# Performance work log

Measured on AMD Instinct MI355X. Metric: run time of the kernel, lower is better.

## Reference

```python
import jax, jax.numpy as jnp
import numpy as np

QLEN, BSZ, HID, NH, HD = 512, 8, 1024, 16, 64
PLEN = 2 * QLEN
SCALE = 1.0 / (HD ** 0.5)
BIG_NUM = 1e30
EPS = 1e-5


def _rel_shift(x, klen):
    # x: [b, n, i, j] -> shifted [b, n, i, klen], same raw-reshape trick as torch.
    b, n, i, j = x.shape
    x = x.reshape(b, n, j, i)[:, :, 1:, :]
    x = x.reshape(b, n, i, j - 1)
    return x[:, :, :, :klen]


def setup_inputs() -> dict:
    key = jax.random.key(0)
    ks = jax.random.split(key, 12)
    s = jnp.float32(0.02)
    return {
        "hidden_states": jax.random.normal(ks[0], (QLEN, BSZ, HID), jnp.float32),
        "position_embed": jax.random.normal(ks[1], (PLEN, BSZ, HID), jnp.float32),
        "segment_embed": jax.random.uniform(ks[2], (QLEN, QLEN, BSZ, 2), jnp.float32),
        "attn_mask": jnp.zeros((QLEN, QLEN, BSZ, 1), jnp.float32),
        "q": jax.random.normal(ks[3], (HID, NH, HD), jnp.float32) * s,
        "k": jax.random.normal(ks[4], (HID, NH, HD), jnp.float32) * s,
        "v": jax.random.normal(ks[5], (HID, NH, HD), jnp.float32) * s,
        "r": jax.random.normal(ks[6], (HID, NH, HD), jnp.float32) * s,
        "o": jax.random.normal(ks[7], (HID, NH, HD), jnp.float32) * s,
        "r_w_bias": jax.random.normal(ks[8], (NH, HD), jnp.float32) * s,
        "r_r_bias": jax.random.normal(ks[9], (NH, HD), jnp.float32) * s,
        "r_s_bias": jax.random.normal(ks[10], (NH, HD), jnp.float32) * s,
        "seg_mat": jax.random.normal(ks[11], (2, NH, HD), jnp.float32) * s,
        "ln_gamma": jnp.ones((HID,), jnp.float32),
        "ln_beta": jnp.zeros((HID,), jnp.float32),
    }


def reference(hidden_states, position_embed, segment_embed, attn_mask,
              q, k, v, r, o, r_w_bias, r_r_bias, r_s_bias, seg_mat,
              ln_gamma, ln_beta):
    query = jnp.einsum('ibh,hnd->ibnd', hidden_states, q)
    key_ = jnp.einsum('ibh,hnd->ibnd', hidden_states, k)
    value = jnp.einsum('ibh,hnd->ibnd', hidden_states, v)
    key_r = jnp.einsum('ibh,hnd->ibnd', position_embed, r)

    # content score
    ac = jnp.einsum('ibnd,jbnd->bnij', query + r_w_bias, key_)
    # relative position score with rel_shift
    bd = jnp.einsum('ibnd,jbnd->bnij', query + r_r_bias, key_r)
    bd = _rel_shift(bd, ac.shape[3])
    # segment score
    ef = jnp.einsum('ibnd,snd->ibns', query + r_s_bias, seg_mat)
    ef = jnp.einsum('ijbs,ibns->bnij', segment_embed, ef)

    attn_score = (ac + bd + ef) * SCALE
    attn_score = attn_score - BIG_NUM * jnp.transpose(attn_mask, (2, 3, 0, 1))
    attn_prob = jax.nn.softmax(attn_score, axis=-1)  # dropout is identity in eval

    attn_out = jnp.einsum('bnij,jbnd->ibnd', attn_prob, value)
    attn_out = jnp.einsum('ibnd,hnd->ibh', attn_out, o)

    x = attn_out + hidden_states
    mu = jnp.mean(x, axis=-1, keepdims=True)
    var = jnp.mean((x - mu) ** 2, axis=-1, keepdims=True)
    return (x - mu) * jax.lax.rsqrt(var + EPS) * ln_gamma + ln_beta
```

## Files before the change

kernel.cpp:

```cpp
#include <hip/hip_runtime.h>
#include <hip/hip_bf16.h>

#define I_LEN 512
#define BSZ   8
#define HIDN  1024
#define NHEAD 16
#define HDIM  64
#define PLEN_ 1024
#define SCALE_F 0.125f
#define BIGNUM 1e30f
#define LN_EPS 1e-5f

typedef unsigned int   u32;
typedef unsigned short u16;
typedef __attribute__((ext_vector_type(8))) short bf16x8;
typedef __attribute__((ext_vector_type(4))) float f32x4;

__device__ __forceinline__ float bflo(u32 w) { return __uint_as_float(w << 16); }
__device__ __forceinline__ float bfhi(u32 w) { return __uint_as_float(w & 0xffff0000u); }
__device__ __forceinline__ u16 f2bf(float x) {
  u32 u = __float_as_uint(x);
  return (u16)((u + 0x7fffu + ((u >> 16) & 1u)) >> 16);
}
__device__ __forceinline__ void bf8_to_f(const uint4 v, float* f) {
  f[0] = bflo(v.x); f[1] = bfhi(v.x);
  f[2] = bflo(v.y); f[3] = bfhi(v.y);
  f[4] = bflo(v.z); f[5] = bfhi(v.z);
  f[6] = bflo(v.w); f[7] = bfhi(v.w);
}

#define GLOAD_LDS16(gp, lp) __builtin_amdgcn_global_load_lds( \
    (const __attribute__((address_space(1))) void*)(gp),      \
    (__attribute__((address_space(3))) void*)(lp), 16, 0, 0)

__device__ __forceinline__ void setrans_body(int i, int j,
    const float* __restrict__ sege, const float* __restrict__ amask,
    u16* __restrict__ SE4, u16* __restrict__ MK) {
  const float* sp = &sege[((size_t)i * 512 + j) * 16];
  const float* mp = &amask[((size_t)i * 512 + j) * 8];
  float se[16], mk[8];
#pragma unroll
  for (int q = 0; q < 4; ++q) {
    const float4 f = *(const float4*)(sp + q * 4);
    se[q * 4 + 0] = f.x; se[q * 4 + 1] = f.y; se[q * 4 + 2] = f.z; se[q * 4 + 3] = f.w;
  }
#pragma unroll
  for (int q = 0; q < 2; ++q) {
    const float4 f = *(const float4*)(mp + q * 4);
    mk[q * 4 + 0] = f.x; mk[q * 4 + 1] = f.y; mk[q * 4 + 2] = f.z; mk[q * 4 + 3] = f.w;
  }
#pragma unroll
  for (int b = 0; b < 8; ++b) {
    const u32 pk = (u32)f2bf(se[b * 2]) | ((u32)f2bf(se[b * 2 + 1]) << 16);
    const size_t plane = ((size_t)b * 512 + i) * 512 + j;
    *(u32*)&SE4[plane * 2] = pk;
    MK[plane] = f2bf(BIGNUM * mk[b]);
  }
}

__global__ __launch_bounds__(256)
void prep_kernel(const float* __restrict__ W0, const float* __restrict__ W1,
                 const float* __restrict__ W2, const float* __restrict__ W3,
                 u16* __restrict__ T0, u16* __restrict__ T1,
                 u16* __restrict__ T2, u16* __restrict__ T3,
                 const float* __restrict__ hidden, const float* __restrict__ ow,
                 u16* __restrict__ Hb, u16* __restrict__ Wob,
                 const float* __restrict__ sege, const float* __restrict__ amask,
                 u16* __restrict__ SE4, u16* __restrict__ MK,
                 const float* __restrict__ pos, u16* __restrict__ Pb) {
  const int blk = blockIdx.x;
  const int t = threadIdx.x;
  if (blk >= 4608) {
    const size_t off = ((size_t)(blk - 4608) * 256 + t) * 8;
    const float4 a = *(const float4*)&pos[off];
    const float4 b = *(const float4*)&pos[off + 4];
    ushort4 o0, o1;
    o0.x = f2bf(a.x); o0.y = f2bf(a.y); o0.z = f2bf(a.z); o0.w = f2bf(a.w);
    o1.x = f2bf(b.x); o1.y = f2bf(b.y); o1.z = f2bf(b.z); o1.w = f2bf(b.w);
    *(ushort4*)&Pb[off] = o0;
    *(ushort4*)&Pb[off + 4] = o1;
    return;
  }
  if (blk >= 3584) {
    const int sid = blk - 3584;
    setrans_body(sid & 511, (sid >> 9) * 256 + t, sege, amask, SE4, MK);
    return;
  }
  if (blk >= 1024) {
    const size_t i = (size_t)(blk - 1024) * 256 + t;
    const float* src; u16* dst; size_t off;
    if (i < 524288) { src = hidden; dst = Hb;  off = i * 8; }
    else            { src = ow;     dst = Wob; off = (i - 524288) * 8; }
    const float4 a = *(const float4*)&src[off];
    const float4 b = *(const float4*)&src[off + 4];
    ushort4 o0, o1;
    o0.x = f2bf(a.x); o0.y = f2bf(a.y); o0.z = f2bf(a.z); o0.w = f2bf(a.w);
    o1.x = f2bf(b.x); o1.y = f2bf(b.y); o1.z = f2bf(b.z); o1.w = f2bf(b.w);
    *(ushort4*)&dst[off] = o0;
    *(ushort4*)&dst[off + 4] = o1;
    return;
  }
  __shared__ u16 tile[64][72];
  const int x = blk & 15, y = (blk >> 4) & 15, z = blk >> 8;
  const float* W = (z == 0) ? W0 : ((z == 1) ? W1 : ((z == 2) ? W2 : W3));
  u16* T = (z == 0) ? T0 : ((z == 1) ? T1 : ((z == 2) ? T2 : T3));
  const int h0 = y * 64, nd0 = x * 64;
  {
    const int hr = t >> 2, c0 = (t & 3) * 16;
#pragma unroll
    for (int q = 0; q < 4; ++q) {
      const float4 f = *(const float4*)&W[(size_t)(h0 + hr) * 1024 + nd0 + c0 + q * 4];
      tile[hr][c0 + q * 4 + 0] = f2bf(f.x);
      tile[hr][c0 + q * 4 + 1] = f2bf(f.y);
      tile[hr][c0 + q * 4 + 2] = f2bf(f.z);
      tile[hr][c0 + q * 4 + 3] = f2bf(f.w);
    }
  }
  __syncthreads();
  const int ndr = t >> 2, hc0 = (t & 3) * 16;
  union { u16 us[16]; uint4 qv[2]; } o;
#pragma unroll
  for (int e = 0; e < 16; ++e) o.us[e] = tile[hc0 + e][ndr];
  uint4* dst = (uint4*)&T[(size_t)(nd0 + ndr) * 1024 + h0 + hc0];
  dst[0] = o.qv[0]; dst[1] = o.qv[1];
}

__global__ __launch_bounds__(256)
void proj_gemm(const u16* __restrict__ Hb, const float* __restrict__ pos,
               const u16* __restrict__ Pb,
               const u16* __restrict__ Wqt, const u16* __restrict__ Wkt,
               const u16* __restrict__ Wvt, const u16* __restrict__ Wrt,
               u16* __restrict__ Qh, u16* __restrict__ Kf,
               u16* __restrict__ Vh, u16* __restrict__ Krf) {
  constexpr int K = 1024;
  __shared__ union {
    struct { u16 As[2 * 8192]; u16 Bs[2 * 8192]; } st;
    u16 epi[4][64 * 68];
    u16 epiK[128 * 137];
  } sm;
  u16* As = sm.st.As;
  u16* Bs = sm.st.Bs;
  const int id = blockIdx.x;
  const int low = id & 7;
  const int rest = id >> 3;
  const int bx = rest & 7;
  const int grp = low + 8 * (rest >> 3);
  const int by = grp & 31;
  const int z = grp >> 5;
  const u16* Bt; u16* C;
  if (z == 0)      { Bt = Wqt; C = Qh;  }
  else if (z == 1) { Bt = Wkt; C = Kf;  }
  else if (z == 2) { Bt = Wvt; C = Vh;  }
  else if (z == 3) { Bt = Wrt; C = Krf; }
  else             { Bt = Wrt; C = Krf; }
  const int rowoff = (z == 4) ? 4096 : 0;
  const float* Apos = pos + (size_t)rowoff * 1024;
  const u16* A16 = (z < 3) ? Hb : (Pb ? Pb + (size_t)rowoff * 1024 : nullptr);
  const int bm = by * 128, bn = bx * 128;
  const int tid = threadIdx.x, wv = tid >> 6, lane = tid & 63;
  const int l15 = lane & 15, g = lane >> 4;
  const int wr = wv >> 1, wc = wv & 1;

#define STAGE_B_P(BUF, K0)                                                    \
  _Pragma("unroll")                                                           \
  for (int p = 0; p < 4; ++p) {                                               \
    const int unit = (wv * 4 + p) * 64 + lane;                                \
    const int row = unit >> 3, up = unit & 7, cc = up ^ (row & 7);            \
    GLOAD_LDS16(&Bt[(size_t)(bn + row) * K + (K0) + cc * 8],                  \
                &Bs[(BUF) * 8192 + unit * 8]);                                \
  }
#define STAGE_A16_P(BUF, K0)                                                  \
  _Pragma("unroll")                                                           \
  for (int p = 0; p < 4; ++p) {                                               \
    const int unit = (wv * 4 + p) * 64 + lane;                                \
    const int row = unit >> 3, up = unit & 7, cc = up ^ (row & 7);            \
    GLOAD_LDS16(&A16[(size_t)(bm + row) * K + (K0) + cc * 8],                 \
                &As[(BUF) * 8192 + unit * 8]);                                \
  }
#define STAGE_A32_P(BUF, K0)                                                  \
  _Pragma("unroll")                                                           \
  for (int p = 0; p < 4; ++p) {                                               \
    const int unit = p * 256 + tid;                                           \
    const int row = unit >> 3, up = unit & 7, cc = up ^ (row & 7);            \
    const float* src = &Apos[(size_t)(bm + row) * K + (K0) + cc * 8];         \
    const float4 f0 = *(const float4*)src;                                    \
    const float4 f1 = *(const float4*)(src + 4);                              \
    ushort4 h0, h1;                                                           \
    h0.x = f2bf(f0.x); h0.y = f2bf(f0.y); h0.z = f2bf(f0.z); h0.w = f2bf(f0.w); \
    h1.x = f2bf(f1.x); h1.y = f2bf(f1.y); h1.z = f2bf(f1.z); h1.w = f2bf(f1.w); \
    *(ushort4*)&As[(BUF) * 8192 + unit * 8] = h0;                             \
    *(ushort4*)&As[(BUF) * 8192 + unit * 8 + 4] = h1;                         \
  }
#define COMPUTE_TILE(CUR)                                                     \
  {                                                                           \
    const u16* Ac = &As[(CUR) * 8192];                                        \
    const u16* Bc = &Bs[(CUR) * 8192];                                        \
    _Pragma("unroll")                                                         \
    for (int h = 0; h < 2; ++h) {                                             \
      bf16x8 af[4], bfv[4];                                                   \
      _Pragma("unroll")                                                       \
      for (int m = 0; m < 4; ++m) {                                           \
        const int row = wr * 64 + m * 16 + l15;                               \
        af[m] = *(const bf16x8*)&Ac[row * 64 + ((h * 4 + g) ^ (row & 7)) * 8];\
      }                                                                       \
      _Pragma("unroll")                                                       \
      for (int n = 0; n < 4; ++n) {                                           \
        const int col = wc * 64 + n * 16 + l15;                               \
        bfv[n] = *(const bf16x8*)&Bc[col * 64 + ((h * 4 + g) ^ (col & 7)) * 8];\
      }                                                                       \
      _Pragma("unroll")                                                       \
      for (int m = 0; m < 4; ++m)                                             \
        _Pragma("unroll")                                                     \
        for (int n = 0; n < 4; ++n)                                           \
          acc[m][n] = __builtin_amdgcn_mfma_f32_16x16x32_bf16(af[m], bfv[n],  \
                                                              acc[m][n], 0, 0, 0); \
    }                                                                         \
  }

  f32x4 acc[4][4];
#pragma unroll
  for (int m = 0; m < 4; ++m)
#pragma unroll
    for (int n = 0; n < 4; ++n) acc[m][n] = (f32x4){0.f, 0.f, 0.f, 0.f};

  if (A16) {
    STAGE_B_P(0, 0);
    STAGE_A16_P(0, 0);
    int cur = 0;
    for (int t = 0; t < 16; ++t) {
      if (t < 15) {
        const int k1 = (t + 1) * 64;
        STAGE_B_P(cur ^ 1, k1);
        STAGE_A16_P(cur ^ 1, k1);
        asm volatile("s_waitcnt vmcnt(8)" ::: "memory");
      } else {
        asm volatile("s_waitcnt vmcnt(0)" ::: "memory");
      }
      __builtin_amdgcn_s_barrier();
      __builtin_amdgcn_sched_barrier(0);
      COMPUTE_TILE(cur);
      __builtin_amdgcn_s_barrier();
      cur ^= 1;
    }
  } else {
    STAGE_B_P(0, 0);
    STAGE_A32_P(0, 0);
    __syncthreads();
    int cur = 0;
    for (int t = 0; t < 16; ++t) {
      if (t < 15) {
        const int k1 = (t + 1) * 64;
        STAGE_B_P(cur ^ 1, k1);
        STAGE_A32_P(cur ^ 1, k1);
      }
      COMPUTE_TILE(cur);
      __syncthreads();
      cur ^= 1;
    }
  }

  if (z == 1 || z >= 3) {
    u16* E128 = sm.epiK;
#pragma unroll
    for (int m = 0; m < 4; ++m)
#pragma unroll
      for (int nf = 0; nf < 4; ++nf)
#pragma unroll
        for (int r = 0; r < 4; ++r)
          E128[(wr * 64 + m * 16 + g * 4 + r) * 137 + wc * 64 + nf * 16 + l15] =
              f2bf(acc[m][nf][r]);
    __syncthreads();
    const int tK = (z == 1) ? by : (by + ((z == 4) ? 32 : 0));
    const int TS = (z == 1) ? 32 : 64;
#pragma unroll
    for (int q = 0; q < 8; ++q) {
      const int rid = wv * 8 + q;
      const int n_loc = rid >> 4, b_ = (rid >> 1) & 7, h = rid & 1;
      union { u16 us[8]; uint4 qv; } o;
#pragma unroll
      for (int e = 0; e < 8; ++e)
        o.us[e] = E128[(l15 * 8 + b_) * 137 + n_loc * 64 + h * 32 + g * 8 + e];
      const int head = bx * 2 + n_loc;
      const size_t base = (((size_t)(b_ * 16 + head) * TS + tK) * 2 + h) * 512 + lane * 8;
      *(uint4*)&C[base] = o.qv;
    }
  } else {
    u16* slice = sm.epi[wv];
    __syncthreads();
#pragma unroll
    for (int m = 0; m < 4; ++m)
#pragma unroll
      for (int nf = 0; nf < 4; ++nf)
#pragma unroll
        for (int r = 0; r < 4; ++r)
          slice[(m * 16 + g * 4 + r) * 68 + nf * 16 + l15] = f2bf(acc[m][nf][r]);
#pragma unroll
    for (int it = 0; it < 8; ++it) {
      const int rl = it * 8 + (lane >> 3);
      const int cl = (lane & 7) * 8;
      const ushort4 a = *(const ushort4*)&slice[rl * 68 + cl];
      const ushort4 b2 = *(const ushort4*)&slice[rl * 68 + cl + 4];
      const int row = bm + wr * 64 + rl;
      const int col = bn + wc * 64 + cl;
      const size_t idx = ((size_t)((row & 7) * 16 + (col >> 6)) * 512 + (row >> 3)) * 64 + (col & 63);
      *(ushort4*)&C[idx] = a;
      *(ushort4*)&C[idx + 4] = b2;
    }
  }
}

__global__ __launch_bounds__(256)
void post_kernel(u16* __restrict__ V, const u16* __restrict__ Qh,
                 const float* __restrict__ rsb, const float* __restrict__ segm,
                 float* __restrict__ E) {
  const int blk = blockIdx.x;
  const int t = threadIdx.x;
  if (blk >= 1024) {
    const int gt = (blk - 1024) * 256 + t;
    const int i = gt >> 7, bb = (gt >> 4) & 7, n = gt & 15;
    const size_t base = (((size_t)bb * 16 + n) * 512 + i) * 64;
    float e0 = 0.f, e1 = 0.f;
#pragma unroll
    for (int u8 = 0; u8 < 8; ++u8) {
      const uint4 qv = *(const uint4*)&Qh[base + u8 * 8];
      float qf[8];
      bf8_to_f(qv, qf);
#pragma unroll
      for (int w = 0; w < 8; ++w) {
        const int d = u8 * 8 + w;
        const float q = qf[w] + rsb[n * HDIM + d];
        e0 += q * segm[n * HDIM + d];
        e1 += q * segm[HIDN + n * HDIM + d];
      }
    }
    E[(size_t)gt * 2 + 0] = e0;
    E[(size_t)gt * 2 + 1] = e1;
    return;
  }
  __shared__ u16 tile[64][72];
  const int bn = blk & 127, slab = blk >> 7;
  const size_t base = ((size_t)bn * 8 + slab) * 4096;
  {
    const int jl = t >> 2, c0 = (t & 3) * 16;
    const uint4 v0 = *(const uint4*)&V[base + jl * 64 + c0];
    const uint4 v1 = *(const uint4*)&V[base + jl * 64 + c0 + 8];
    *(uint4*)&tile[jl][c0] = v0;
    *(uint4*)&tile[jl][c0 + 8] = v1;
  }
  __syncthreads();
  const int lane = t & 63, g = lane >> 4, l15 = lane & 15;
#pragma unroll
  for (int w = 0; w < 2; ++w) {
    const int run = w * 4 + (t >> 6);
    const int c = run >> 1, h = run & 1;
    union { u16 us[8]; uint4 qv; } o;
#pragma unroll
    for (int e = 0; e < 8; ++e) o.us[e] = tile[h * 32 + g * 8 + e][16 * c + l15];
    *(uint4*)&V[base + run * 512 + lane * 8] = o.qv;
  }
}

__global__ __launch_bounds__(256)
void attn_mfma(const u16* __restrict__ Qh, const u16* __restrict__ Kf,
               const u16* __restrict__ Vf, const u16* __restrict__ Krf,
               const float* __restrict__ E, const u16* __restrict__ SE4,
               const u16* __restrict__ MK, const float* __restrict__ rwb,
               const float* __restrict__ rrb, u16* __restrict__ AOb) {
  __shared__ u16 Pl[4][16 * 64];
  const int id = blockIdx.x;
  const int b = id & 7, n = (id >> 3) & 15;
  const int i0 = (id >> 7) * 64;
  const int bn = b * 16 + n;
  const int t = threadIdx.x, wv = t >> 6, lane = t & 63;
  const int l15 = lane & 15, g = lane >> 4;
  const int irow0 = i0 + wv * 16;
  u16* Pw = Pl[wv];
  const int bn64 = bn * 64;

  bf16x8 qcf[2], qrf[2];
#pragma unroll
  for (int h = 0; h < 2; ++h) {
    const int d0 = 32 * h + g * 8;
    const uint4 qv = *(const uint4*)&Qh[((size_t)bn * 512 + irow0 + l15) * 64 + d0];
    float qf[8]; bf8_to_f(qv, qf);
    union { u16 us[8]; bf16x8 v; } ua, ub;
#pragma unroll
    for (int w = 0; w < 8; ++w) {
      ua.us[w] = f2bf((qf[w] + rwb[n * HDIM + d0 + w]) * SCALE_F);
      ub.us[w] = f2bf((qf[w] + rrb[n * HDIM + d0 + w]) * SCALE_F);
    }
    qcf[h] = ua.v; qrf[h] = ub.v;
  }

  float e0v[4], e1v[4], lrun[4];
  f32x4 accO[4];
#pragma unroll
  for (int r = 0; r < 4; ++r) {
    const int i = irow0 + 4 * g + r;
    const float2 ee = *(const float2*)&E[((size_t)(i * BSZ + b) * NHEAD + n) * 2];
    e0v[r] = ee.x * SCALE_F; e1v[r] = ee.y * SCALE_F;
    lrun[r] = 0.f;
  }
#pragma unroll
  for (int c = 0; c < 4; ++c) accO[c] = (f32x4){0.f, 0.f, 0.f, 0.f};

  for (int jb = 0; jb < I_LEN; jb += 64) {
    u32 sev[4][4]; u16 mkv[4][4];
#pragma unroll
    for (int c = 0; c < 4; ++c)
#pragma unroll
      for (int r = 0; r < 4; ++r) {
        const size_t plane = ((size_t)b * 512 + (irow0 + 4 * g + r)) * 512 + jb + 16 * c + l15;
        sev[c][r] = *(const u32*)&SE4[plane * 2];
        mkv[c][r] = MK[plane];
      }
    bf16x8 vf[4][2];
#pragma unroll
    for (int c = 0; c < 4; ++c) {
      const u16* vp = &Vf[((((size_t)bn * 8 + (jb >> 6)) * 4 + c) * 2) * 512 + lane * 8];
      vf[c][0] = *(const bf16x8*)vp;
      vf[c][1] = *(const bf16x8*)(vp + 512);
    }
    f32x4 S[4];
#pragma unroll
    for (int c = 0; c < 4; ++c) S[c] = (f32x4){0.f, 0.f, 0.f, 0.f};
#pragma unroll
    for (int c = 0; c < 4; ++c) {
      const u16* kp = &Kf[(((size_t)bn * 32 + (jb >> 4) + c) * 2) * 512 + lane * 8];
      S[c] = __builtin_amdgcn_mfma_f32_16x16x32_bf16(qcf[0], *(const bf16x8*)kp, S[c], 0, 0, 0);
      S[c] = __builtin_amdgcn_mfma_f32_16x16x32_bf16(qcf[1], *(const bf16x8*)(kp + 512), S[c], 0, 0, 0);
    }
    const int tb = (jb + 496 - irow0) >> 4;
    f32x4 T[5];
#pragma unroll
    for (int c = 0; c < 5; ++c) T[c] = (f32x4){0.f, 0.f, 0.f, 0.f};
#pragma unroll
    for (int c = 0; c < 5; ++c) {
      const u16* kp = &Krf[(((size_t)bn * 64 + tb + c) * 2) * 512 + lane * 8];
      T[c] = __builtin_amdgcn_mfma_f32_16x16x32_bf16(qrf[0], *(const bf16x8*)kp, T[c], 0, 0, 0);
      T[c] = __builtin_amdgcn_mfma_f32_16x16x32_bf16(qrf[1], *(const bf16x8*)(kp + 512), T[c], 0, 0, 0);
    }
    float bd[4][4];
#pragma unroll
    for (int r = 0; r < 4; ++r) {
      const int ii = 4 * g + r;
      const int pos_ = (lane & 48) | ((l15 - ii) & 15);
      float bp[5];
#pragma unroll
      for (int c = 0; c < 5; ++c) bp[c] = __shfl(T[c][r], pos_, 64);
      const bool sel = l15 >= ii;
#pragma unroll
      for (int c = 0; c < 4; ++c) bd[c][r] = sel ? bp[c + 1] : bp[c];
    }
#pragma unroll
    for (int c = 0; c < 4; ++c)
#pragma unroll
      for (int r = 0; r < 4; ++r) {
        const u32 sev_ = sev[c][r];
        const float s = S[c][r] + bd[c][r] + bflo(sev_) * e0v[r] + bfhi(sev_) * e1v[r]
                        - bflo((u32)mkv[c][r]);
        const float p = __expf(s);
        S[c][r] = p;
        lrun[r] += p;
      }
#pragma unroll
    for (int c = 0; c < 4; ++c)
#pragma unroll
      for (int r = 0; r < 4; ++r) {
        const int ii = 4 * g + r;
        Pw[ii * 64 + ((16 * c + l15) ^ ((ii & 7) << 3))] = f2bf(S[c][r]);
      }
    const bf16x8 pa0 = *(const bf16x8*)&Pw[l15 * 64 + ((g * 8) ^ ((l15 & 7) << 3))];
    const bf16x8 pa1 = *(const bf16x8*)&Pw[l15 * 64 + ((32 + g * 8) ^ ((l15 & 7) << 3))];
#pragma unroll
    for (int c = 0; c < 4; ++c) {
      accO[c] = __builtin_amdgcn_mfma_f32_16x16x32_bf16(pa0, vf[c][0], accO[c], 0, 0, 0);
      accO[c] = __builtin_amdgcn_mfma_f32_16x16x32_bf16(pa1, vf[c][1], accO[c], 0, 0, 0);
    }
  }
#pragma unroll
  for (int r = 0; r < 4; ++r) {
#pragma unroll
    for (int o = 1; o < 16; o <<= 1) lrun[r] += __shfl_xor(lrun[r], o);
  }
#pragma unroll
  for (int c = 0; c < 4; ++c)
#pragma unroll
    for (int r = 0; r < 4; ++r) {
      const int ii = 4 * g + r;
      AOb[(size_t)(irow0 + ii) * 8192 + bn64 + 16 * c + l15] = f2bf(accO[c][r] / lrun[r]);
    }
}

__global__ __launch_bounds__(256)
void oproj_gemm(const u16* __restrict__ A, const u16* __restrict__ Wob,
                const float* __restrict__ Res, float* __restrict__ C) {
  constexpr int K = 1024;
  __shared__ u16 As[2 * 4096];
  __shared__ u16 Bs[2 * 8192];
  const int id = blockIdx.x;
  const int low = id & 7;
  const int rest = id >> 3;
  const int bx = rest & 7;
  const int by = low + 8 * (rest >> 3);
  const int bm = by * 64, bn = bx * 128;
  const int tid = threadIdx.x, wv = tid >> 6, lane = tid & 63;
  const int l15 = lane & 15, g = lane >> 4;
  const int wr = wv >> 1, wc = wv & 1;

#define STAGE_O(BUF, K0)                                                      \
  _Pragma("unroll")                                                           \
  for (int p = 0; p < 2; ++p) {                                               \
    const int unit = (wv * 2 + p) * 64 + lane;                                \
    const int row = unit >> 3, up = unit & 7, cc = up ^ (row & 7);            \
    GLOAD_LDS16(&A[(size_t)(bm + row) * K + (K0) + cc * 8],                   \
                &As[(BUF) * 4096 + unit * 8]);                                \
  }                                                                           \
  _Pragma("unroll")                                                           \
  for (int p = 0; p < 4; ++p) {                                               \
    const int unit = (wv * 4 + p) * 64 + lane;                                \
    const int row = unit >> 3, up = unit & 7, cc = up ^ (row & 7);            \
    GLOAD_LDS16(&Wob[(size_t)(bn + row) * K + (K0) + cc * 8],                 \
                &Bs[(BUF) * 8192 + unit * 8]);                                \
  }

  f32x4 acc[2][4];
#pragma unroll
  for (int m = 0; m < 2; ++m)
#pragma unroll
    for (int n = 0; n < 4; ++n) acc[m][n] = (f32x4){0.f, 0.f, 0.f, 0.f};

  STAGE_O(0, 0);
  int cur = 0;
  for (int t = 0; t < 16; ++t) {
    if (t < 15) {
      STAGE_O(cur ^ 1, (t + 1) * 64);
      asm volatile("s_waitcnt vmcnt(6)" ::: "memory");
    } else {
      asm volatile("s_waitcnt vmcnt(0)" ::: "memory");
    }
    __builtin_amdgcn_s_barrier();
    __builtin_amdgcn_sched_barrier(0);
    const u16* Ac = &As[cur * 4096];
    const u16* Bc = &Bs[cur * 8192];
#pragma unroll
    for (int h = 0; h < 2; ++h) {
      bf16x8 af[2], bfv[4];
#pragma unroll
      for (int m = 0; m < 2; ++m) {
        const int row = wr * 32 + m * 16 + l15;
        af[m] = *(const bf16x8*)&Ac[row * 64 + ((h * 4 + g) ^ (row & 7)) * 8];
      }
#pragma unroll
      for (int n = 0; n < 4; ++n) {
        const int col = wc * 64 + n * 16 + l15;
        bfv[n] = *(const bf16x8*)&Bc[col * 64 + ((h * 4 + g) ^ (col & 7)) * 8];
      }
#pragma unroll
      for (int m = 0; m < 2; ++m)
#pragma unroll
        for (int n = 0; n < 4; ++n)
          acc[m][n] = __builtin_amdgcn_mfma_f32_16x16x32_bf16(af[m], bfv[n], acc[m][n], 0, 0, 0);
    }
    __builtin_amdgcn_s_barrier();
    cur ^= 1;
  }
#pragma unroll
  for (int m = 0; m < 2; ++m) {
    const int row0 = bm + wr * 32 + m * 16 + g * 4;
#pragma unroll
    for (int nf = 0; nf < 4; ++nf) {
      const int col = bn + wc * 64 + nf * 16 + l15;
#pragma unroll
      for (int r = 0; r < 4; ++r) {
        const int row = row0 + r;
        C[(size_t)row * 1024 + col] = acc[m][nf][r] + Res[(size_t)row * 1024 + col];
      }
    }
  }
}

__global__ __launch_bounds__(256)
void ln_kernel(const float* __restrict__ X, const float* __restrict__ gam,
               const float* __restrict__ bet, float* __restrict__ out) {
  const int row = blockIdx.x, t = threadIdx.x;
  const float4 x4 = *(const float4*)&X[(size_t)row * HIDN + t * 4];
  float s  = x4.x + x4.y + x4.z + x4.w;
  float sq = x4.x * x4.x + x4.y * x4.y + x4.z * x4.z + x4.w * x4.w;
#pragma unroll
  for (int o = 32; o >= 1; o >>= 1) { s += __shfl_xor(s, o); sq += __shfl_xor(sq, o); }
  __shared__ float red[8];
  const int wv = t >> 6;
  if ((t & 63) == 0) { red[wv * 2] = s; red[wv * 2 + 1] = sq; }
  __syncthreads();
  s  = red[0] + red[2] + red[4] + red[6];
  sq = red[1] + red[3] + red[5] + red[7];
  const float mu  = s * (1.f / HIDN);
  const float var = sq * (1.f / HIDN) - mu * mu;
  const float rs  = rsqrtf(var + LN_EPS);
  const float4 g4 = *(const float4*)&gam[t * 4];
  const float4 b4 = *(const float4*)&bet[t * 4];
  float4 o4;
  o4.x = (x4.x - mu) * rs * g4.x + b4.x;
  o4.y = (x4.y - mu) * rs * g4.y + b4.y;
  o4.z = (x4.z - mu) * rs * g4.z + b4.z;
  o4.w = (x4.w - mu) * rs * g4.w + b4.w;
  *(float4*)&out[(size_t)row * HIDN + t * 4] = o4;
}

extern "C" void kernel_launch(void* const* d_in, const int* in_sizes, int n_in,
                              void* d_out, int out_size, void* d_ws, size_t ws_size,
                              hipStream_t stream) {
  (void)in_sizes; (void)n_in; (void)out_size;
  const float* hidden = (const float*)d_in[0];
  const float* pos    = (const float*)d_in[1];
  const float* sege   = (const float*)d_in[2];
  const float* amask  = (const float*)d_in[3];
  const float* qw     = (const float*)d_in[4];
  const float* kw     = (const float*)d_in[5];
  const float* vw     = (const float*)d_in[6];
  const float* rw     = (const float*)d_in[7];
  const float* ow     = (const float*)d_in[8];
  const float* rwb    = (const float*)d_in[9];
  const float* rrb    = (const float*)d_in[10];
  const float* rsb    = (const float*)d_in[11];
  const float* segm   = (const float*)d_in[12];
  const float* gam    = (const float*)d_in[13];
  const float* bet    = (const float*)d_in[14];
  float* out = (float*)d_out;
  char* ws = (char*)d_ws;

  const size_t MiB = 1ull << 20;
  u16*   Wqt = (u16*)(ws);
  u16*   Wkt = (u16*)(ws + 2 * MiB);
  u16*   Wvt = (u16*)(ws + 4 * MiB);
  u16*   Wrt = (u16*)(ws + 6 * MiB);
  u16*   AOb = (u16*)(ws);
  u16*   Qh  = (u16*)(ws + 8 * MiB);
  u16*   Kf  = (u16*)(ws + 16 * MiB);
  u16*   Vf  = (u16*)(ws + 24 * MiB);
  u16*   Krf = (u16*)(ws + 32 * MiB);
  float* X   = (float*)(ws + 32 * MiB);
  u16*   Hb  = (u16*)(ws + 48 * MiB);
  u16*   MK  = (u16*)(ws + 56 * MiB);
  float* E   = (float*)(ws + 60 * MiB);
  u16*   Wob = (u16*)(ws + 60 * MiB + 512 * 1024);
  u16*   SE4 = (u16*)(ws + 62 * MiB + 512 * 1024);
  const bool fullTier = ws_size >= (86 * MiB + 512 * 1024 + 4096);
  u16*   Pb  = fullTier ? (u16*)(ws + 70 * MiB + 512 * 1024) : nullptr;

  prep_kernel<<<fullTier ? 8704 : 4608, 256, 0, stream>>>(
      qw, kw, vw, rw, Wqt, Wkt, Wvt, Wrt, hidden, ow, Hb, Wob,
      sege, amask, SE4, MK, pos, Pb);
  proj_gemm<<<1280, 256, 0, stream>>>(Hb, pos, Pb, Wqt, Wkt, Wvt, Wrt,
                                      Qh, Kf, Vf, Krf);
  post_kernel<<<1280, 256, 0, stream>>>(Vf, Qh, rsb, segm, E);
  attn_mfma<<<1024, 256, 0, stream>>>(Qh, Kf, Vf, Krf, E, SE4, MK, rwb, rrb, AOb);
  oproj_gemm<<<512, 256, 0, stream>>>(AOb, Wob, hidden, X);
  ln_kernel<<<4096, 256, 0, stream>>>(X, gam, bet, out);
}
```

Before: 161.3 us.

## Process two 16-row query tiles per wave in attention, reusing K fragments; use exp2

Each wave in the attention kernel now handles 32 query rows as two 16-row sub-tiles, so the content-key fragments loaded per 64-column block are shared by both sub-tiles, and the grid is halved to 512 blocks. The softmax exponent moves to base 2: the scale, segment factors and mask are premultiplied by log2(e) and the hardware exp2 builtin replaces __expf. MFMA sections are wrapped in s_setprio to favour matrix issue. The cost is more registers per wave and fewer blocks in flight (512 blocks on a large GPU), which may lower occupancy and latency hiding.

```diff
diff --git a/kernel.cpp b/kernel.cpp
--- a/kernel.cpp
+++ b/kernel.cpp
@@ -10,6 +10,7 @@
 #define SCALE_F 0.125f
 #define BIGNUM 1e30f
 #define LN_EPS 1e-5f
+#define L2E_F 1.44269504f
 
 typedef unsigned int   u32;
 typedef unsigned short u16;
@@ -54,7 +55,7 @@
     const u32 pk = (u32)f2bf(se[b * 2]) | ((u32)f2bf(se[b * 2 + 1]) << 16);
     const size_t plane = ((size_t)b * 512 + i) * 512 + j;
     *(u32*)&SE4[plane * 2] = pk;
-    MK[plane] = f2bf(BIGNUM * mk[b]);
+    MK[plane] = f2bf(L2E_F * BIGNUM * mk[b]);
   }
 }
 
@@ -369,127 +370,152 @@
   __shared__ u16 Pl[4][16 * 64];
   const int id = blockIdx.x;
   const int b = id & 7, n = (id >> 3) & 15;
-  const int i0 = (id >> 7) * 64;
+  const int i0 = (id >> 7) * 128;
   const int bn = b * 16 + n;
   const int t = threadIdx.x, wv = t >> 6, lane = t & 63;
   const int l15 = lane & 15, g = lane >> 4;
-  const int irow0 = i0 + wv * 16;
+  const int irow0 = i0 + wv * 32;
   u16* Pw = Pl[wv];
   const int bn64 = bn * 64;
-
-  bf16x8 qcf[2], qrf[2];
-#pragma unroll
-  for (int h = 0; h < 2; ++h) {
-    const int d0 = 32 * h + g * 8;
-    const uint4 qv = *(const uint4*)&Qh[((size_t)bn * 512 + irow0 + l15) * 64 + d0];
-    float qf[8]; bf8_to_f(qv, qf);
-    union { u16 us[8]; bf16x8 v; } ua, ub;
-#pragma unroll
-    for (int w = 0; w < 8; ++w) {
-      ua.us[w] = f2bf((qf[w] + rwb[n * HDIM + d0 + w]) * SCALE_F);
-      ub.us[w] = f2bf((qf[w] + rrb[n * HDIM + d0 + w]) * SCALE_F);
-    }
-    qcf[h] = ua.v; qrf[h] = ub.v;
-  }
-
-  float e0v[4], e1v[4], lrun[4];
-  f32x4 accO[4];
-#pragma unroll
-  for (int r = 0; r < 4; ++r) {
-    const int i = irow0 + 4 * g + r;
-    const float2 ee = *(const float2*)&E[((size_t)(i * BSZ + b) * NHEAD + n) * 2];
-    e0v[r] = ee.x * SCALE_F; e1v[r] = ee.y * SCALE_F;
-    lrun[r] = 0.f;
-  }
-#pragma unroll
-  for (int c = 0; c < 4; ++c) accO[c] = (f32x4){0.f, 0.f, 0.f, 0.f};
+  const float SC = SCALE_F * L2E_F;
+
+  bf16x8 qcf[2][2], qrf[2][2];
+#pragma unroll
+  for (int mm = 0; mm < 2; ++mm)
+#pragma unroll
+    for (int h = 0; h < 2; ++h) {
+      const int d0 = 32 * h + g * 8;
+      const uint4 qv = *(const uint4*)&Qh[((size_t)bn * 512 + irow0 + mm * 16 + l15) * 64 + d0];
+      float qf[8]; bf8_to_f(qv, qf);
+      union { u16 us[8]; bf16x8 v; } ua, ub;
+#pragma unroll
+      for (int w = 0; w < 8; ++w) {
+        ua.us[w] = f2bf((qf[w] + rwb[n * HDIM + d0 + w]) * SC);
+        ub.us[w] = f2bf((qf[w] + rrb[n * HDIM + d0 + w]) * SC);
+      }
+      qcf[mm][h] = ua.v; qrf[mm][h] = ub.v;
+    }
+
+  float e0v[2][4], e1v[2][4], lrun[2][4];
+  f32x4 accO[2][4];
+#pragma unroll
+  for (int mm = 0; mm < 2; ++mm)
+#pragma unroll
+    for (int r = 0; r < 4; ++r) {
+      const int i = irow0 + mm * 16 + 4 * g + r;
+      const float2 ee = *(const float2*)&E[((size_t)(i * BSZ + b) * NHEAD + n) * 2];
+      e0v[mm][r] = ee.x * SC; e1v[mm][r] = ee.y * SC;
+      lrun[mm][r] = 0.f;
+    }
+#pragma unroll
+  for (int mm = 0; mm < 2; ++mm)
+#pragma unroll
+    for (int c = 0; c < 4; ++c) accO[mm][c] = (f32x4){0.f, 0.f, 0.f, 0.f};
 
   for (int jb = 0; jb < I_LEN; jb += 64) {
-    u32 sev[4][4]; u16 mkv[4][4];
-#pragma unroll
-    for (int c = 0; c < 4; ++c)
-#pragma unroll
-      for (int r = 0; r < 4; ++r) {
-        const size_t plane = ((size_t)b * 512 + (irow0 + 4 * g + r)) * 512 + jb + 16 * c + l15;
-        sev[c][r] = *(const u32*)&SE4[plane * 2];
-        mkv[c][r] = MK[plane];
-      }
-    bf16x8 vf[4][2];
-#pragma unroll
-    for (int c = 0; c < 4; ++c) {
-      const u16* vp = &Vf[((((size_t)bn * 8 + (jb >> 6)) * 4 + c) * 2) * 512 + lane * 8];
-      vf[c][0] = *(const bf16x8*)vp;
-      vf[c][1] = *(const bf16x8*)(vp + 512);
-    }
-    f32x4 S[4];
-#pragma unroll
-    for (int c = 0; c < 4; ++c) S[c] = (f32x4){0.f, 0.f, 0.f, 0.f};
+    bf16x8 kf[4][2];
 #pragma unroll
     for (int c = 0; c < 4; ++c) {
       const u16* kp = &Kf[(((size_t)bn * 32 + (jb >> 4) + c) * 2) * 512 + lane * 8];
-      S[c] = __builtin_amdgcn_mfma_f32_16x16x32_bf16(qcf[0], *(const bf16x8*)kp, S[c], 0, 0, 0);
-      S[c] = __builtin_amdgcn_mfma_f32_16x16x32_bf16(qcf[1], *(const bf16x8*)(kp + 512), S[c], 0, 0, 0);
-    }
-    const int tb = (jb + 496 - irow0) >> 4;
-    f32x4 T[5];
-#pragma unroll
-    for (int c = 0; c < 5; ++c) T[c] = (f32x4){0.f, 0.f, 0.f, 0.f};
-#pragma unroll
-    for (int c = 0; c < 5; ++c) {
-      const u16* kp = &Krf[(((size_t)bn * 64 + tb + c) * 2) * 512 + lane * 8];
-      T[c] = __builtin_amdgcn_mfma_f32_16x16x32_bf16(qrf[0], *(const bf16x8*)kp, T[c], 0, 0, 0);
-      T[c] = __builtin_amdgcn_mfma_f32_16x16x32_bf16(qrf[1], *(const bf16x8*)(kp + 512), T[c], 0, 0, 0);
-    }
-    float bd[4][4];
-#pragma unroll
-    for (int r = 0; r < 4; ++r) {
-      const int ii = 4 * g + r;
-      const int pos_ = (lane & 48) | ((l15 - ii) & 15);
-      float bp[5];
-#pragma unroll
-      for (int c = 0; c < 5; ++c) bp[c] = __shfl(T[c][r], pos_, 64);
-      const bool sel = l15 >= ii;
-#pragma unroll
-      for (int c = 0; c < 4; ++c) bd[c][r] = sel ? bp[c + 1] : bp[c];
-    }
-#pragma unroll
-    for (int c = 0; c < 4; ++c)
-#pragma unroll
-      for (int r = 0; r < 4; ++r) {
-        const u32 sev_ = sev[c][r];
-        const float s = S[c][r] + bd[c][r] + bflo(sev_) * e0v[r] + bfhi(sev_) * e1v[r]
-                        - bflo((u32)mkv[c][r]);
-        const float p = __expf(s);
-        S[c][r] = p;
-        lrun[r] += p;
-      }
-#pragma unroll
-    for (int c = 0; c < 4; ++c)
+      kf[c][0] = *(const bf16x8*)kp;
+      kf[c][1] = *(const bf16x8*)(kp + 512);
+    }
+#pragma unroll
+    for (int mm = 0; mm < 2; ++mm) {
+      const int irm = irow0 + mm * 16;
+      f32x4 S[4];
+#pragma unroll
+      for (int c = 0; c < 4; ++c) S[c] = (f32x4){0.f, 0.f, 0.f, 0.f};
+      __builtin_amdgcn_s_setprio(1);
+#pragma unroll
+      for (int c = 0; c < 4; ++c) {
+        S[c] = __builtin_amdgcn_mfma_f32_16x16x32_bf16(qcf[mm][0], kf[c][0], S[c], 0, 0, 0);
+        S[c] = __builtin_amdgcn_mfma_f32_16x16x32_bf16(qcf[mm][1], kf[c][1], S[c], 0, 0, 0);
+      }
+      __builtin_amdgcn_s_setprio(0);
+      const int tb = (jb + 496 - irm) >> 4;
+      f32x4 T[5];
+#pragma unroll
+      for (int c = 0; c < 5; ++c) T[c] = (f32x4){0.f, 0.f, 0.f, 0.f};
+#pragma unroll
+      for (int c = 0; c < 5; ++c) {
+        const u16* kp = &Krf[(((size_t)bn * 64 + tb + c) * 2) * 512 + lane * 8];
+        T[c] = __builtin_amdgcn_mfma_f32_16x16x32_bf16(qrf[mm][0], *(const bf16x8*)kp, T[c], 0, 0, 0);
+        T[c] = __builtin_amdgcn_mfma_f32_16x16x32_bf16(qrf[mm][1], *(const bf16x8*)(kp + 512), T[c], 0, 0, 0);
+      }
+      u32 sev[4][4]; u16 mkv[4][4];
+#pragma unroll
+      for (int c = 0; c < 4; ++c)
+#pragma unroll
+        for (int r = 0; r < 4; ++r) {
+          const size_t plane = ((size_t)b * 512 + (irm + 4 * g + r)) * 512 + jb + 16 * c + l15;
+          sev[c][r] = *(const u32*)&SE4[plane * 2];
+          mkv[c][r] = MK[plane];
+        }
+      bf16x8 vf[4][2];
+#pragma unroll
+      for (int c = 0; c < 4; ++c) {
+        const u16* vp = &Vf[((((size_t)bn * 8 + (jb >> 6)) * 4 + c) * 2) * 512 + lane * 8];
+        vf[c][0] = *(const bf16x8*)vp;
+        vf[c][1] = *(const bf16x8*)(vp + 512);
+      }
+      float bd[4][4];
 #pragma unroll
       for (int r = 0; r < 4; ++r) {
         const int ii = 4 * g + r;
-        Pw[ii * 64 + ((16 * c + l15) ^ ((ii & 7) << 3))] = f2bf(S[c][r]);
-      }
-    const bf16x8 pa0 = *(const bf16x8*)&Pw[l15 * 64 + ((g * 8) ^ ((l15 & 7) << 3))];
-    const bf16x8 pa1 = *(const bf16x8*)&Pw[l15 * 64 + ((32 + g * 8) ^ ((l15 & 7) << 3))];
-#pragma unroll
-    for (int c = 0; c < 4; ++c) {
-      accO[c] = __builtin_amdgcn_mfma_f32_16x16x32_bf16(pa0, vf[c][0], accO[c], 0, 0, 0);
-      accO[c] = __builtin_amdgcn_mfma_f32_16x16x32_bf16(pa1, vf[c][1], accO[c], 0, 0, 0);
-    }
-  }
-#pragma unroll
-  for (int r = 0; r < 4; ++r) {
-#pragma unroll
-    for (int o = 1; o < 16; o <<= 1) lrun[r] += __shfl_xor(lrun[r], o);
-  }
-#pragma unroll
-  for (int c = 0; c < 4; ++c)
+        const int pos_ = (lane & 48) | ((l15 - ii) & 15);
+        float bp[5];
+#pragma unroll
+        for (int c = 0; c < 5; ++c) bp[c] = __shfl(T[c][r], pos_, 64);
+        const bool sel = l15 >= ii;
+#pragma unroll
+        for (int c = 0; c < 4; ++c) bd[c][r] = sel ? bp[c + 1] : bp[c];
+      }
+#pragma unroll
+      for (int c = 0; c < 4; ++c)
+#pragma unroll
+        for (int r = 0; r < 4; ++r) {
+          const u32 sev_ = sev[c][r];
+          const float s = S[c][r] + bd[c][r] + bflo(sev_) * e0v[mm][r]
+                          + bfhi(sev_) * e1v[mm][r] - bflo((u32)mkv[c][r]);
+          const float p = __builtin_amdgcn_exp2f(s);
+          S[c][r] = p;
+          lrun[mm][r] += p;
+        }
+#pragma unroll
+      for (int c = 0; c < 4; ++c)
+#pragma unroll
+        for (int r = 0; r < 4; ++r) {
+          const int ii = 4 * g + r;
+          Pw[ii * 64 + ((16 * c + l15) ^ ((ii & 7) << 3))] = f2bf(S[c][r]);
+        }
+      const bf16x8 pa0 = *(const bf16x8*)&Pw[l15 * 64 + ((g * 8) ^ ((l15 & 7) << 3))];
+      const bf16x8 pa1 = *(const bf16x8*)&Pw[l15 * 64 + ((32 + g * 8) ^ ((l15 & 7) << 3))];
+      __builtin_amdgcn_s_setprio(1);
+#pragma unroll
+      for (int c = 0; c < 4; ++c) {
+        accO[mm][c] = __builtin_amdgcn_mfma_f32_16x16x32_bf16(pa0, vf[c][0], accO[mm][c], 0, 0, 0);
+        accO[mm][c] = __builtin_amdgcn_mfma_f32_16x16x32_bf16(pa1, vf[c][1], accO[mm][c], 0, 0, 0);
+      }
+      __builtin_amdgcn_s_setprio(0);
+    }
+  }
+#pragma unroll
+  for (int mm = 0; mm < 2; ++mm) {
 #pragma unroll
     for (int r = 0; r < 4; ++r) {
-      const int ii = 4 * g + r;
-      AOb[(size_t)(irow0 + ii) * 8192 + bn64 + 16 * c + l15] = f2bf(accO[c][r] / lrun[r]);
-    }
+#pragma unroll
+      for (int o = 1; o < 16; o <<= 1) lrun[mm][r] += __shfl_xor(lrun[mm][r], o);
+    }
+#pragma unroll
+    for (int c = 0; c < 4; ++c)
+#pragma unroll
+      for (int r = 0; r < 4; ++r) {
+        const int ii = 4 * g + r;
+        AOb[(size_t)(irow0 + mm * 16 + ii) * 8192 + bn64 + 16 * c + l15] =
+            f2bf(accO[mm][c][r] / lrun[mm][r]);
+      }
+  }
 }
 
 __global__ __launch_bounds__(256)
@@ -655,7 +681,7 @@
   proj_gemm<<<1280, 256, 0, stream>>>(Hb, pos, Pb, Wqt, Wkt, Wvt, Wrt,
                                       Qh, Kf, Vf, Krf);
   post_kernel<<<1280, 256, 0, stream>>>(Vf, Qh, rsb, segm, E);
-  attn_mfma<<<1024, 256, 0, stream>>>(Qh, Kf, Vf, Krf, E, SE4, MK, rwb, rrb, AOb);
+  attn_mfma<<<512, 256, 0, stream>>>(Qh, Kf, Vf, Krf, E, SE4, MK, rwb, rrb, AOb);
   oproj_gemm<<<512, 256, 0, stream>>>(AOb, Wob, hidden, X);
   ln_kernel<<<4096, 256, 0, stream>>>(X, gam, bet, out);
 }
```

Result: slower. 244.2 us (+51.4%).
